# Performance work log

Hardware: AMD Instinct MI355X
Metric: run time of the kernel (lower is better)

## Reference

```python
import jax, jax.numpy as jnp
import numpy as np

# dims: T timesteps (=window_size[0]), B_ = num_windows*batch, window 8x8, C=dim
T, B, WH, WW, C, NH = 4, 1024, 8, 8, 256, 8
HD = C // NH          # head_dim = 32
N = T * WH * WW       # tokens per window volume = 256
V_TH, TAU, ALPHA = 1.0, 2.0, 4.0  # LIF threshold, membrane tau, surrogate sharpness

@jax.custom_vjp
def spike(v):
    # Heaviside spike with sigmoid surrogate gradient (standard spikingjelly-style)
    return (v >= 0.0).astype(v.dtype)

def _spike_fwd(v):
    return spike(v), v

def _spike_bwd(v, g):
    sg = jax.nn.sigmoid(ALPHA * v)
    return (g * ALPHA * sg * (1.0 - sg),)

spike.defvjp(_spike_fwd, _spike_bwd)

def lif(x):
    """Multi-step LIF neuron over leading time axis. x: (T, ...). Hard reset to 0."""
    def step(v, xt):
        v = v + (xt - v) / TAU
        s = spike(v - V_TH)
        return v * (1.0 - s), s
    _, s = jax.lax.scan(step, jnp.zeros_like(x[0]), x)
    return s

def setup_inputs() -> dict:
    key = jax.random.key(0)
    ks = jax.random.split(key, 6)
    sc = 1.0 / np.sqrt(C)
    return {
        "x":   jax.random.normal(ks[0], (T, B, WH, WW, C), jnp.float32),
        "Wq":  jax.random.normal(ks[1], (C, C), jnp.float32) * sc,   # linear_q weight (no bias)
        "Wk":  jax.random.normal(ks[2], (C, C), jnp.float32) * sc,   # linear_k weight (no bias)
        "Wp":  jax.random.normal(ks[3], (C, C), jnp.float32) * sc,   # proj weight
        "bp":  jnp.zeros((C,), jnp.float32),                         # proj bias
        "pos": jax.random.normal(ks[4], (1, NH, N, HD), jnp.float32) * 0.02,  # positional_encoding param
    }

def reference(x, Wq, Wk, Wp, bp, pos):
    # proj_sn on raw input
    xs = lif(x)                                        # (T,B,WH,WW,C) spikes
    # Q path: linear -> spiking neuron (norm=None branch skipped)
    q = lif(xs @ Wq.T)                                 # (T,B,WH,WW,C)
    # K path: linear -> add positional encoding -> spiking neuron
    k = lif(xs @ Wk.T + pos.reshape(T, 1, WH, WW, C))  # (T,B,WH,WW,C)
    # head split exactly as torch reshapes (row-major, mixes T into B for k)
    q = q.reshape(T, B, NH, WH * WW, HD)
    k = k.reshape(B, NH, T * WH * WW, HD)
    # token attention: sum over head_dim, spike, elementwise multiply with k
    att_token = lif(q.sum(-1, keepdims=True))          # (T,B,NH,HW,1)
    attn = k * att_token.reshape(B, NH, -1, 1)         # (B,NH,T*HW,HD)
    # exact torch permute/reshape back to (T,B,WH,WW,C)
    x2 = attn.reshape(B, NH, T, WH, WW, HD).transpose(2, 0, 3, 4, 1, 5).reshape(T, B, WH, WW, C)
    attn_out = lif(x2)                                 # attn_sn output (second return value)
    y = (x2 @ Wp.T + bp).reshape(B, N, C)              # proj then final reshape (B_, N, C)
    return y, attn_out
```

## Files before the change

### kernel.cpp

```cpp
#include <hip/hip_runtime.h>
#include <hip/hip_bf16.h>

static constexpr int  G     = 65536;
static constexpr long PLANE = 16777216L;

__device__ __forceinline__ float bfh(unsigned short u) {
    union { unsigned u32; float f; } c; c.u32 = ((unsigned)u) << 16; return c.f;
}

__global__ void prep_kernel(const float* __restrict__ Wq, const float* __restrict__ Wk,
                            const float* __restrict__ Wp,
                            __hip_bfloat16* __restrict__ WqT, __hip_bfloat16* __restrict__ WkT,
                            float* __restrict__ WpT, unsigned* __restrict__ flag)
{
    int c = blockIdx.x;
    int j = threadIdx.x;
    int idx = c * 256 + j;
    WqT[idx] = __float2bfloat16(Wq[j * 256 + c]);
    WkT[idx] = __float2bfloat16(Wk[j * 256 + c]);
    WpT[idx] = Wp[j * 256 + c];
    if (c == 0 && j == 0) *flag = 0u;
}

__device__ __forceinline__ void gather_word(unsigned long long mm, int j, int lane,
                                            const __hip_bfloat16* __restrict__ WT,
                                            float& q0, float& q1, float& q2, float& q3)
{
    if (!mm) return;
    int b = __ffsll(mm) - 1; mm &= (mm - 1);
    ushort4 w = *((const ushort4*)(WT + (4 * b + j) * 256 + 4 * lane));
    while (mm) {
        int b2 = __ffsll(mm) - 1; mm &= (mm - 1);
        ushort4 w2 = *((const ushort4*)(WT + (4 * b2 + j) * 256 + 4 * lane));
        q0 += bfh(w.x); q1 += bfh(w.y); q2 += bfh(w.z); q3 += bfh(w.w);
        w = w2;
    }
    q0 += bfh(w.x); q1 += bfh(w.y); q2 += bfh(w.z); q3 += bfh(w.w);
}

__device__ __forceinline__ void gather8(
    unsigned long long m0, unsigned long long m1, unsigned long long m2, unsigned long long m3,
    unsigned long long n0, unsigned long long n1, unsigned long long n2, unsigned long long n3,
    const __hip_bfloat16* __restrict__ WT, int lane,
    float4& qa, float4& qb)
{
    const __hip_bfloat16* base = WT + 4 * lane;
    ushort4 w0 = {0,0,0,0}, w1 = {0,0,0,0}, w2 = {0,0,0,0}, w3 = {0,0,0,0};
    ushort4 x0 = {0,0,0,0}, x1 = {0,0,0,0}, x2 = {0,0,0,0}, x3 = {0,0,0,0};
    while (m0 | m1 | m2 | m3 | n0 | n1 | n2 | n3) {
        bool h0 = m0 != 0, h1 = m1 != 0, h2 = m2 != 0, h3 = m3 != 0;
        bool g0 = n0 != 0, g1 = n1 != 0, g2 = n2 != 0, g3 = n3 != 0;
        if (h0) { int b = __ffsll(m0) - 1; m0 &= m0 - 1; w0 = *(const ushort4*)(base + (4*b+0)*256); }
        if (h1) { int b = __ffsll(m1) - 1; m1 &= m1 - 1; w1 = *(const ushort4*)(base + (4*b+1)*256); }
        if (h2) { int b = __ffsll(m2) - 1; m2 &= m2 - 1; w2 = *(const ushort4*)(base + (4*b+2)*256); }
        if (h3) { int b = __ffsll(m3) - 1; m3 &= m3 - 1; w3 = *(const ushort4*)(base + (4*b+3)*256); }
        if (g0) { int b = __ffsll(n0) - 1; n0 &= n0 - 1; x0 = *(const ushort4*)(base + (4*b+0)*256); }
        if (g1) { int b = __ffsll(n1) - 1; n1 &= n1 - 1; x1 = *(const ushort4*)(base + (4*b+1)*256); }
        if (g2) { int b = __ffsll(n2) - 1; n2 &= n2 - 1; x2 = *(const ushort4*)(base + (4*b+2)*256); }
        if (g3) { int b = __ffsll(n3) - 1; n3 &= n3 - 1; x3 = *(const ushort4*)(base + (4*b+3)*256); }
        if (h0) { qa.x += bfh(w0.x); qa.y += bfh(w0.y); qa.z += bfh(w0.z); qa.w += bfh(w0.w); }
        if (h1) { qa.x += bfh(w1.x); qa.y += bfh(w1.y); qa.z += bfh(w1.z); qa.w += bfh(w1.w); }
        if (h2) { qa.x += bfh(w2.x); qa.y += bfh(w2.y); qa.z += bfh(w2.z); qa.w += bfh(w2.w); }
        if (h3) { qa.x += bfh(w3.x); qa.y += bfh(w3.y); qa.z += bfh(w3.z); qa.w += bfh(w3.w); }
        if (g0) { qb.x += bfh(x0.x); qb.y += bfh(x0.y); qb.z += bfh(x0.z); qb.w += bfh(x0.w); }
        if (g1) { qb.x += bfh(x1.x); qb.y += bfh(x1.y); qb.z += bfh(x1.z); qb.w += bfh(x1.w); }
        if (g2) { qb.x += bfh(x2.x); qb.y += bfh(x2.y); qb.z += bfh(x2.z); qb.w += bfh(x2.w); }
        if (g3) { qb.x += bfh(x3.x); qb.y += bfh(x3.y); qb.z += bfh(x3.z); qb.w += bfh(x3.w); }
    }
}

__global__ __launch_bounds__(256) void lif_qk_kernel(
    const float* __restrict__ x,
    unsigned* __restrict__ AM,
    const __hip_bfloat16* __restrict__ WqT,
    const __hip_bfloat16* __restrict__ WkT,
    const float* __restrict__ pos,
    unsigned* __restrict__ flag)
{
    int lane = threadIdx.x & 63;
    int wv   = threadIdx.x >> 6;
    int wid  = blockIdx.x * 4 + wv;
    int sh   = (lane & 56);

    for (int gi = 0; gi < 4; ++gi) {
        int g  = wid * 4 + gi;
        int hw = g & 63;

        float4 X[4];
        #pragma unroll
        for (int t = 0; t < 4; ++t)
            X[t] = ((const float4*)(x + (long)t * PLANE + (long)g * 256))[lane];

        unsigned long long sm[4][4];
        float4 v = make_float4(0.f, 0.f, 0.f, 0.f);
        #pragma unroll
        for (int t = 0; t < 4; ++t) {
            v.x = v.x + (X[t].x - v.x) * 0.5f; bool s0 = (v.x - 1.0f) >= 0.0f; if (s0) v.x = 0.f;
            v.y = v.y + (X[t].y - v.y) * 0.5f; bool s1 = (v.y - 1.0f) >= 0.0f; if (s1) v.y = 0.f;
            v.z = v.z + (X[t].z - v.z) * 0.5f; bool s2 = (v.z - 1.0f) >= 0.0f; if (s2) v.z = 0.f;
            v.w = v.w + (X[t].w - v.w) * 0.5f; bool s3 = (v.w - 1.0f) >= 0.0f; if (s3) v.w = 0.f;
            sm[t][0] = __ballot(s0);
            sm[t][1] = __ballot(s1);
            sm[t][2] = __ballot(s2);
            sm[t][3] = __ballot(s3);
        }

        float4 qs0 = make_float4(0.f,0.f,0.f,0.f), qs1 = make_float4(0.f,0.f,0.f,0.f);
        float4 qs2 = make_float4(0.f,0.f,0.f,0.f), qs3 = make_float4(0.f,0.f,0.f,0.f);
        gather8(sm[0][0], sm[0][1], sm[0][2], sm[0][3],
                sm[1][0], sm[1][1], sm[1][2], sm[1][3], WqT, lane, qs0, qs1);
        gather8(sm[2][0], sm[2][1], sm[2][2], sm[2][3],
                sm[3][0], sm[3][1], sm[3][2], sm[3][3], WqT, lane, qs2, qs3);

        float4 vq = make_float4(0.f, 0.f, 0.f, 0.f);
        float  va = 0.f;
        unsigned attb = 0u;
        #pragma unroll
        for (int t = 0; t < 4; ++t) {
            float4 q = (t == 0) ? qs0 : (t == 1) ? qs1 : (t == 2) ? qs2 : qs3;
            vq.x = vq.x + (q.x - vq.x) * 0.5f; bool t0 = (vq.x - 1.0f) >= 0.0f; if (t0) vq.x = 0.f;
            vq.y = vq.y + (q.y - vq.y) * 0.5f; bool t1 = (vq.y - 1.0f) >= 0.0f; if (t1) vq.y = 0.f;
            vq.z = vq.z + (q.z - vq.z) * 0.5f; bool t2 = (vq.z - 1.0f) >= 0.0f; if (t2) vq.z = 0.f;
            vq.w = vq.w + (q.w - vq.w) * 0.5f; bool t3 = (vq.w - 1.0f) >= 0.0f; if (t3) vq.w = 0.f;
            unsigned long long qb0 = __ballot(t0);
            unsigned long long qb1 = __ballot(t1);
            unsigned long long qb2 = __ballot(t2);
            unsigned long long qb3 = __ballot(t3);

            int cnt = __popc((unsigned)((qb0 >> sh) & 0xFFull))
                    + __popc((unsigned)((qb1 >> sh) & 0xFFull))
                    + __popc((unsigned)((qb2 >> sh) & 0xFFull))
                    + __popc((unsigned)((qb3 >> sh) & 0xFFull));
            va = va + ((float)cnt - va) * 0.5f;
            bool a = (va - 1.0f) >= 0.0f; if (a) va = 0.f;
            attb |= (a ? 1u : 0u) << t;
        }

        bool anyatt = (__ballot(attb != 0u) != 0ull);
        if (!anyatt) {
            if (lane < 32) {
                int t = lane >> 3, wd = lane & 7;
                AM[((long)t * G + g) * 8 + wd] = 0u;
            }
        } else {
            if (lane == 0) atomicOr(flag, 1u);
            float4 vk = make_float4(0.f, 0.f, 0.f, 0.f);
            #pragma unroll
            for (int t = 0; t < 4; ++t) {
                float k0 = 0.f, k1 = 0.f, k2 = 0.f, k3 = 0.f;
                #pragma unroll
                for (int j = 0; j < 4; ++j)
                    gather_word(sm[t][j], j, lane, WkT, k0, k1, k2, k3);
                float4 pp = ((const float4*)(pos + t * 16384 + hw * 256))[lane];
                k0 += pp.x; k1 += pp.y; k2 += pp.z; k3 += pp.w;

                vk.x = vk.x + (k0 - vk.x) * 0.5f; bool t0 = (vk.x - 1.0f) >= 0.0f; if (t0) vk.x = 0.f;
                vk.y = vk.y + (k1 - vk.y) * 0.5f; bool t1 = (vk.y - 1.0f) >= 0.0f; if (t1) vk.y = 0.f;
                vk.z = vk.z + (k2 - vk.z) * 0.5f; bool t2 = (vk.z - 1.0f) >= 0.0f; if (t2) vk.z = 0.f;
                vk.w = vk.w + (k3 - vk.w) * 0.5f; bool t3 = (vk.w - 1.0f) >= 0.0f; if (t3) vk.w = 0.f;

                bool at = ((attb >> t) & 1u) != 0u;
                unsigned long long bb[4];
                bb[0] = __ballot(t0 && at);
                bb[1] = __ballot(t1 && at);
                bb[2] = __ballot(t2 && at);
                bb[3] = __ballot(t3 && at);
                if (lane < 8) {
                    unsigned wdv = 0u;
                    #pragma unroll
                    for (int hd = 0; hd < 32; ++hd) {
                        int ls = lane * 8 + (hd >> 2);
                        wdv |= (unsigned)((bb[hd & 3] >> ls) & 1ull) << hd;
                    }
                    AM[((long)t * G + g) * 8 + lane] = wdv;
                }
            }
        }
    }
}

__global__ __launch_bounds__(256) void out_kernel(
    const unsigned* __restrict__ AM,
    const float* __restrict__ WpT,
    const float* __restrict__ bp,
    const unsigned* __restrict__ flag,
    float* __restrict__ y,
    float* __restrict__ attn_out)
{
    int lane = threadIdx.x & 63;
    int wv   = threadIdx.x >> 6;
    long wave = (long)blockIdx.x * 4 + wv;
    int  nh   = lane >> 3;

    float4 base = ((const float4*)bp)[lane];
    const float4 z = make_float4(0.f, 0.f, 0.f, 0.f);
    long row0 = wave * 32;

    if (*flag == 0u) {
        float4* yp = (float4*)y        + row0 * 64 + lane;
        float4* ap = (float4*)attn_out + row0 * 64 + lane;
        #pragma unroll 8
        for (int r = 0; r < 32; ++r) yp[r * 64] = base;
        #pragma unroll 8
        for (int r = 0; r < 32; ++r) ap[r * 64] = z;
        return;
    }

    int t2  = (int)(row0 >> 16);
    int b2  = (int)(row0 >> 6) & 1023;
    int hw2 = (int)row0 & 63;
    int srow = (b2 * 4 + (nh >> 1)) * 64 + (nh & 1) * 32 + t2 * 8 + (hw2 >> 3);
    unsigned W = AM[(long)srow * 8 + (hw2 & 7)];

    for (int r = 0; r < 32; ++r) {
        long row = row0 + r;
        unsigned Wn = 0u;
        if (r < 31) {
            long rown = row + 1;
            int t2n  = (int)(rown >> 16);
            int b2n  = (int)(rown >> 6) & 1023;
            int hw2n = (int)rown & 63;
            int srn  = (b2n * 4 + (nh >> 1)) * 64 + (nh & 1) * 32 + t2n * 8 + (hw2n >> 3);
            Wn = AM[(long)srn * 8 + (hw2n & 7)];
        }
        float4 val = base;
        if (__ballot(W != 0u) != 0ull) {
            #pragma unroll 1
            for (int n2 = 0; n2 < 8; ++n2) {
                unsigned Wx = __shfl(W, n2 * 8);
                while (Wx) {
                    int hd = __ffs(Wx) - 1;
                    Wx &= (Wx - 1);
                    float4 wl = ((const float4*)(WpT + (n2 * 32 + hd) * 256))[lane];
                    val.x += wl.x; val.y += wl.y; val.z += wl.z; val.w += wl.w;
                }
            }
        }
        ((float4*)y)[row * 64 + lane]        = val;
        ((float4*)attn_out)[row * 64 + lane] = z;
        W = Wn;
    }
}

extern "C" void kernel_launch(void* const* d_in, const int* in_sizes, int n_in,
                              void* d_out, int out_size, void* d_ws, size_t ws_size,
                              hipStream_t stream) {
    const float* x   = (const float*)d_in[0];
    const float* Wq  = (const float*)d_in[1];
    const float* Wk  = (const float*)d_in[2];
    const float* Wp  = (const float*)d_in[3];
    const float* bp  = (const float*)d_in[4];
    const float* pos = (const float*)d_in[5];

    float* y        = (float*)d_out;
    float* attn_out = y + 67108864L;

    char* ws = (char*)d_ws;
    unsigned*           AM   = (unsigned*)(ws);
    __hip_bfloat16*     WqT  = (__hip_bfloat16*)(ws + (8L << 20));
    __hip_bfloat16*     WkT  = (__hip_bfloat16*)(ws + (8L << 20) + (128L << 10));
    float*              WpT  = (float*)(ws + (8L << 20) + (256L << 10));
    unsigned*           flag = (unsigned*)(ws + (8L << 20) + (512L << 10));

    prep_kernel<<<256, 256, 0, stream>>>(Wq, Wk, Wp, WqT, WkT, WpT, flag);
    lif_qk_kernel<<<4096, 256, 0, stream>>>(x, AM, WqT, WkT, pos, flag);
    out_kernel<<<2048, 256, 0, stream>>>(AM, WpT, bp, flag, y, attn_out);
}
```

Before: 788.9 us.

## Fuse LIF/QK and output projection into one kernel with LDS attention masks

Merges the LIF/Q/K kernel and the output-projection kernel into one kernel of 256 blocks × 1024 threads. Each block computes attention-mask words for 256 window groups into shared memory and then writes the matching y and attn_out rows. This removes the global AM buffer round-trip, the global atomic flag and one launch, and replaces the grid-wide flag with a per-block flag. The cost is only 256 large blocks with 32KB of shared memory each, which lowers occupancy and parallelism on the first phase, and the per-block zero-skip decision is more fragmented.

```diff
diff --git a/kernel.cpp b/kernel.cpp
--- a/kernel.cpp
+++ b/kernel.cpp
@@ -11,7 +11,7 @@
 __global__ void prep_kernel(const float* __restrict__ Wq, const float* __restrict__ Wk,
                             const float* __restrict__ Wp,
                             __hip_bfloat16* __restrict__ WqT, __hip_bfloat16* __restrict__ WkT,
-                            float* __restrict__ WpT, unsigned* __restrict__ flag)
+                            float* __restrict__ WpT)
 {
     int c = blockIdx.x;
     int j = threadIdx.x;
@@ -19,7 +19,6 @@
     WqT[idx] = __float2bfloat16(Wq[j * 256 + c]);
     WkT[idx] = __float2bfloat16(Wk[j * 256 + c]);
     WpT[idx] = Wp[j * 256 + c];
-    if (c == 0 && j == 0) *flag = 0u;
 }
 
 __device__ __forceinline__ void gather_word(unsigned long long mm, int j, int lane,
@@ -69,27 +68,37 @@
     }
 }
 
-__global__ __launch_bounds__(256) void lif_qk_kernel(
+__global__ __launch_bounds__(1024) void fused_kernel(
     const float* __restrict__ x,
-    unsigned* __restrict__ AM,
     const __hip_bfloat16* __restrict__ WqT,
     const __hip_bfloat16* __restrict__ WkT,
+    const float* __restrict__ WpT,
+    const float* __restrict__ bp,
     const float* __restrict__ pos,
-    unsigned* __restrict__ flag)
-{
+    float* __restrict__ y,
+    float* __restrict__ attn_out)
+{
+    __shared__ unsigned AMs[1024 * 8];
+    __shared__ unsigned anyflag;
+
+    int p    = blockIdx.x;
     int lane = threadIdx.x & 63;
     int wv   = threadIdx.x >> 6;
-    int wid  = blockIdx.x * 4 + wv;
     int sh   = (lane & 56);
-
-    for (int gi = 0; gi < 4; ++gi) {
-        int g  = wid * 4 + gi;
-        int hw = g & 63;
+    long g0  = (long)p * 256;
+
+    if (threadIdx.x == 0) anyflag = 0u;
+    __syncthreads();
+
+    for (int gi = 0; gi < 16; ++gi) {
+        int  tl = wv * 16 + gi;
+        long g  = g0 + tl;
+        int  hw = (int)g & 63;
 
         float4 X[4];
         #pragma unroll
         for (int t = 0; t < 4; ++t)
-            X[t] = ((const float4*)(x + (long)t * PLANE + (long)g * 256))[lane];
+            X[t] = ((const float4*)(x + (long)t * PLANE + g * 256))[lane];
 
         unsigned long long sm[4][4];
         float4 v = make_float4(0.f, 0.f, 0.f, 0.f);
@@ -140,10 +149,10 @@
         if (!anyatt) {
             if (lane < 32) {
                 int t = lane >> 3, wd = lane & 7;
-                AM[((long)t * G + g) * 8 + wd] = 0u;
+                AMs[(t * 256 + tl) * 8 + wd] = 0u;
             }
         } else {
-            if (lane == 0) atomicOr(flag, 1u);
+            if (lane == 0) anyflag = 1u;
             float4 vk = make_float4(0.f, 0.f, 0.f, 0.f);
             #pragma unroll
             for (int t = 0; t < 4; ++t) {
@@ -172,73 +181,43 @@
                         int ls = lane * 8 + (hd >> 2);
                         wdv |= (unsigned)((bb[hd & 3] >> ls) & 1ull) << hd;
                     }
-                    AM[((long)t * G + g) * 8 + lane] = wdv;
+                    AMs[(t * 256 + tl) * 8 + lane] = wdv;
                 }
             }
         }
     }
-}
-
-__global__ __launch_bounds__(256) void out_kernel(
-    const unsigned* __restrict__ AM,
-    const float* __restrict__ WpT,
-    const float* __restrict__ bp,
-    const unsigned* __restrict__ flag,
-    float* __restrict__ y,
-    float* __restrict__ attn_out)
-{
-    int lane = threadIdx.x & 63;
-    int wv   = threadIdx.x >> 6;
-    long wave = (long)blockIdx.x * 4 + wv;
-    int  nh   = lane >> 3;
-
+
+    __syncthreads();
+
+    int tt = wv >> 2;
+    int t2 = wv & 3;
+    long rowbase = (long)t2 * 65536 + ((long)tt * 256 + p) * 64;
+    float4* yp = (float4*)y        + rowbase * 64 + lane;
+    float4* ap = (float4*)attn_out + rowbase * 64 + lane;
     float4 base = ((const float4*)bp)[lane];
     const float4 z = make_float4(0.f, 0.f, 0.f, 0.f);
-    long row0 = wave * 32;
-
-    if (*flag == 0u) {
-        float4* yp = (float4*)y        + row0 * 64 + lane;
-        float4* ap = (float4*)attn_out + row0 * 64 + lane;
+
+    if (anyflag == 0u) {
         #pragma unroll 8
-        for (int r = 0; r < 32; ++r) yp[r * 64] = base;
+        for (int i = 0; i < 64; ++i) yp[i * 64] = base;
         #pragma unroll 8
-        for (int r = 0; r < 32; ++r) ap[r * 64] = z;
-        return;
-    }
-
-    int t2  = (int)(row0 >> 16);
-    int b2  = (int)(row0 >> 6) & 1023;
-    int hw2 = (int)row0 & 63;
-    int srow = (b2 * 4 + (nh >> 1)) * 64 + (nh & 1) * 32 + t2 * 8 + (hw2 >> 3);
-    unsigned W = AM[(long)srow * 8 + (hw2 & 7)];
-
-    for (int r = 0; r < 32; ++r) {
-        long row = row0 + r;
-        unsigned Wn = 0u;
-        if (r < 31) {
-            long rown = row + 1;
-            int t2n  = (int)(rown >> 16);
-            int b2n  = (int)(rown >> 6) & 1023;
-            int hw2n = (int)rown & 63;
-            int srn  = (b2n * 4 + (nh >> 1)) * 64 + (nh & 1) * 32 + t2n * 8 + (hw2n >> 3);
-            Wn = AM[(long)srn * 8 + (hw2n & 7)];
-        }
-        float4 val = base;
-        if (__ballot(W != 0u) != 0ull) {
+        for (int i = 0; i < 64; ++i) ap[i * 64] = z;
+    } else {
+        for (int i = 0; i < 64; ++i) {
+            float4 val = base;
             #pragma unroll 1
-            for (int n2 = 0; n2 < 8; ++n2) {
-                unsigned Wx = __shfl(W, n2 * 8);
-                while (Wx) {
-                    int hd = __ffs(Wx) - 1;
-                    Wx &= (Wx - 1);
-                    float4 wl = ((const float4*)(WpT + (n2 * 32 + hd) * 256))[lane];
+            for (int nh = 0; nh < 8; ++nh) {
+                unsigned W = AMs[(tt * 256 + (nh >> 1) * 64 + (nh & 1) * 32 + t2 * 8 + (i >> 3)) * 8 + (i & 7)];
+                while (W) {
+                    int hd = __ffs(W) - 1;
+                    W &= (W - 1);
+                    float4 wl = ((const float4*)WpT)[(nh * 32 + hd) * 64 + lane];
                     val.x += wl.x; val.y += wl.y; val.z += wl.z; val.w += wl.w;
                 }
             }
-        }
-        ((float4*)y)[row * 64 + lane]        = val;
-        ((float4*)attn_out)[row * 64 + lane] = z;
-        W = Wn;
+            yp[i * 64] = val;
+            ap[i * 64] = z;
+        }
     }
 }
 
@@ -256,13 +235,10 @@
     float* attn_out = y + 67108864L;
 
     char* ws = (char*)d_ws;
-    unsigned*           AM   = (unsigned*)(ws);
-    __hip_bfloat16*     WqT  = (__hip_bfloat16*)(ws + (8L << 20));
-    __hip_bfloat16*     WkT  = (__hip_bfloat16*)(ws + (8L << 20) + (128L << 10));
-    float*              WpT  = (float*)(ws + (8L << 20) + (256L << 10));
-    unsigned*           flag = (unsigned*)(ws + (8L << 20) + (512L << 10));
-
-    prep_kernel<<<256, 256, 0, stream>>>(Wq, Wk, Wp, WqT, WkT, WpT, flag);
-    lif_qk_kernel<<<4096, 256, 0, stream>>>(x, AM, WqT, WkT, pos, flag);
-    out_kernel<<<2048, 256, 0, stream>>>(AM, WpT, bp, flag, y, attn_out);
-}
+    __hip_bfloat16* WqT = (__hip_bfloat16*)(ws);
+    __hip_bfloat16* WkT = (__hip_bfloat16*)(ws + (128L << 10));
+    float*          WpT = (float*)(ws + (256L << 10));
+
+    prep_kernel<<<256, 256, 0, stream>>>(Wq, Wk, Wp, WqT, WkT, WpT);
+    fused_kernel<<<256, 1024, 0, stream>>>(x, WqT, WkT, WpT, bp, pos, y, attn_out);
+}
```

Result: slower. 806.2 us (+2.2%).
